# Kernel tuning notes

Hardware: AMD Instinct MI355X
Metric: run time of the kernel (lower is better)

Reference implementation:

```python
import jax, jax.numpy as jnp
import numpy as np

# LeNet C3 sparse connection table derived from the TF loop logic:
#   outputs 0-5 : 3 consecutive input channels (i, i+1, i+2 mod 6)  -> weights3[:,:,m,i]
#   outputs 6-11: 4 consecutive input channels (k..k+3 mod 6)       -> weights4[:,:,m,k]
#   outputs 12-14: channels (k, k+1, k+3, k+4 mod 6)                -> weights4_4[:,:,m,k]
#   output 15  : all 6 channels                                     -> weights6
# Missing connections contribute exactly zero, so assembling one dense
# [f,f,6,16] kernel with zeros in unconnected slots and running a single
# VALID conv computes the SAME math as the ~60 tiny conv2d calls.

BATCH, H, W, CIN, COUT, FS = 32, 512, 512, 6, 16, 5


def setup_inputs() -> dict:
    key = jax.random.key(0)
    k1, k2, k3, k4, k5, k6 = jax.random.split(key, 6)
    return {
        "inputs": jax.random.normal(k1, (BATCH, H, W, CIN), dtype=jnp.float32),
        "weights3": jax.random.normal(k2, (FS, FS, 3, 6), dtype=jnp.float32),
        "weights4": jax.random.normal(k3, (FS, FS, 4, 6), dtype=jnp.float32),
        "weights4_4": jax.random.normal(k4, (FS, FS, 4, 3), dtype=jnp.float32),
        "weights6": jax.random.normal(k5, (FS, FS, 6, 1), dtype=jnp.float32),
        "bias1": jax.random.normal(k6, (COUT,), dtype=jnp.float32),
    }


def _dense_kernel(weights3, weights4, weights4_4, weights6):
    f = weights3.shape[0]
    Wd = jnp.zeros((f, f, CIN, COUT), dtype=weights3.dtype)
    # outputs 0..5: 3 consecutive channels
    for i in range(6):
        for m in range(3):
            Wd = Wd.at[:, :, (i + m) % 6, i].set(weights3[:, :, m, i])
    # outputs 6..11: 4 consecutive channels
    for k in range(6):
        for m in range(4):
            Wd = Wd.at[:, :, (k + m) % 6, 6 + k].set(weights4[:, :, m, k])
    # outputs 12..14: offsets 0,1,3,4
    for k in range(3):
        for m, off in enumerate((0, 1, 3, 4)):
            Wd = Wd.at[:, :, (k + off) % 6, 12 + k].set(weights4_4[:, :, m, k])
    # output 15: all 6 channels
    Wd = Wd.at[:, :, :, 15].set(weights6[:, :, :, 0])
    return Wd


def reference(inputs, weights3, weights4, weights4_4, weights6, bias1):
    Wd = _dense_kernel(weights3, weights4, weights4_4, weights6)
    out = jax.lax.conv_general_dilated(
        inputs, Wd, window_strides=(1, 1), padding="VALID",
        dimension_numbers=("NHWC", "HWIO", "NHWC"))
    return out + bias1  # broadcast bias over [B, H', W', 16]
```

## Files before the change

### kernel.cpp

```cpp
#include <hip/hip_runtime.h>
#include <cstddef>

namespace {
constexpr int kBatch = 32, kH = 512, kW = 512, kCin = 6, kCout = 16, kFs = 5;
constexpr int kOH = kH - kFs + 1, kOW = kW - kFs + 1;
constexpr int kTile = 32;
constexpr int kIT = kTile + kFs - 1;
constexpr int kRowB = kIT * kCin;
constexpr int kWElems = kFs * kFs * kCin * kCout;
}

__global__ void assemble_weights(const float* __restrict__ w3,
                                 const float* __restrict__ w4,
                                 const float* __restrict__ w44,
                                 const float* __restrict__ w6,
                                 float* __restrict__ wd) {
  int i = blockIdx.x * blockDim.x + threadIdx.x;
  if (i >= kWElems) return;
  int o = i & 15;
  int c = (i >> 4) % kCin;
  int p = i / (kCout * kCin);
  float val = 0.f;
  if (o < 6) {
    int m = (c - o + 6) % 6;
    if (m < 3) val = w3[(p * 3 + m) * 6 + o];
  } else if (o < 12) {
    int k = o - 6;
    int m = (c - k + 6) % 6;
    if (m < 4) val = w4[(p * 4 + m) * 6 + k];
  } else if (o < 15) {
    int k = o - 12;
    int d = (c - k + 6) % 6;
    int m = (d == 0) ? 0 : (d == 1) ? 1 : (d == 3) ? 2 : (d == 4) ? 3 : -1;
    if (m >= 0) val = w44[(p * 4 + m) * 3 + k];
  } else {
    val = w6[p * 6 + c];
  }
  wd[i] = val;
}

#define FMA16(P)                                                                      \
  {                                                                                   \
    float v = s_in[(ty + ((P) >> 1) * 16 + ky) * kRowB + (tx + ((P)&1) * 16 + kx) * kCin + c]; \
    acc[P][0].x += v * w0.x; acc[P][0].y += v * w0.y; acc[P][0].z += v * w0.z; acc[P][0].w += v * w0.w; \
    acc[P][1].x += v * w1.x; acc[P][1].y += v * w1.y; acc[P][1].z += v * w1.z; acc[P][1].w += v * w1.w; \
    acc[P][2].x += v * w2.x; acc[P][2].y += v * w2.y; acc[P][2].z += v * w2.z; acc[P][2].w += v * w2.w; \
    acc[P][3].x += v * w3.x; acc[P][3].y += v * w3.y; acc[P][3].z += v * w3.z; acc[P][3].w += v * w3.w; \
  }

__global__ __launch_bounds__(256) void conv_sparse(
    const float* __restrict__ in, const float* __restrict__ wd,
    const float* __restrict__ bias, float* __restrict__ out) {
  __shared__ float s_in[kIT * kRowB];
  __shared__ float s_w[kWElems];

  const int t = threadIdx.x;
  const int bx0 = blockIdx.x * kTile, by0 = blockIdx.y * kTile;
  const int b = blockIdx.z;

  for (int i = t; i < kWElems; i += 256) s_w[i] = wd[i];

  const float* inb = in + (size_t)b * kH * kW * kCin;
  const bool interior = (bx0 + kIT <= kW) && (by0 + kIT <= kH);
  if (interior) {
    for (int i = t; i < kIT * kRowB; i += 256) {
      int r = i / kRowB;
      int rem = i - r * kRowB;
      s_in[i] = inb[((size_t)(by0 + r) * kW + bx0) * kCin + rem];
    }
  } else {
    for (int i = t; i < kIT * kRowB; i += 256) {
      int r = i / kRowB;
      int rem = i - r * kRowB;
      int gy = by0 + r;
      int gx = bx0 + rem / kCin;
      float v = 0.f;
      if (gy < kH && gx < kW) v = inb[((size_t)gy * kW + bx0) * kCin + rem];
      s_in[i] = v;
    }
  }
  __syncthreads();

  const int tx = t & 15, ty = t >> 4;

  const float4* bp = (const float4*)bias;
  float4 b0 = bp[0], b1 = bp[1], b2 = bp[2], b3 = bp[3];
  float4 acc[4][4];
#pragma unroll
  for (int p = 0; p < 4; ++p) {
    acc[p][0] = b0; acc[p][1] = b1; acc[p][2] = b2; acc[p][3] = b3;
  }

#pragma unroll 1
  for (int ky = 0; ky < kFs; ++ky) {
#pragma unroll
    for (int kx = 0; kx < kFs; ++kx) {
#pragma unroll
      for (int c = 0; c < kCin; ++c) {
        const float4* wp = (const float4*)&s_w[((ky * kFs + kx) * kCin + c) * kCout];
        float4 w0 = wp[0], w1 = wp[1], w2 = wp[2], w3 = wp[3];
        FMA16(0)
        FMA16(1)
        FMA16(2)
        FMA16(3)
      }
    }
  }

#pragma unroll
  for (int p = 0; p < 4; ++p) {
    int oy = by0 + ty + (p >> 1) * 16;
    int ox = bx0 + tx + (p & 1) * 16;
    if (oy < kOH && ox < kOW) {
      float4* op = (float4*)&out[(((size_t)b * kOH + oy) * kOW + ox) * kCout];
      op[0] = acc[p][0]; op[1] = acc[p][1]; op[2] = acc[p][2]; op[3] = acc[p][3];
    }
  }
}

extern "C" void kernel_launch(void* const* d_in, const int* in_sizes, int n_in,
                              void* d_out, int out_size, void* d_ws, size_t ws_size,
                              hipStream_t stream) {
  const float* in   = (const float*)d_in[0];
  const float* w3   = (const float*)d_in[1];
  const float* w4   = (const float*)d_in[2];
  const float* w44  = (const float*)d_in[3];
  const float* w6   = (const float*)d_in[4];
  const float* bias = (const float*)d_in[5];
  float* out = (float*)d_out;
  float* wd  = (float*)d_ws;

  assemble_weights<<<(kWElems + 255) / 256, 256, 0, stream>>>(w3, w4, w44, w6, wd);

  dim3 grid((kOW + kTile - 1) / kTile, (kOH + kTile - 1) / kTile, kBatch);
  conv_sparse<<<grid, 256, 0, stream>>>(in, wd, bias, out);
}
```

Measured before the change: 1.022 ms.

## Skip zero weights via static connection table and read weights from global

The inner loop now uses a compile-time per-input-channel table of the 10 connected output channels, so only the nonzero weight slots are multiplied instead of all 16. That cuts FMAs to about 60 of the original 96 per pixel and tap. Weights are now read straight from global memory (uniform scalar loads) rather than staged in shared memory. Interior input tiles are loaded as float4 and the input pairs as float2. The risks are more scalar and global weight loads inside the hot loop and possibly higher register pressure.

```diff
diff --git a/kernel.cpp b/kernel.cpp
--- a/kernel.cpp
+++ b/kernel.cpp
@@ -8,6 +8,17 @@
 constexpr int kIT = kTile + kFs - 1;
 constexpr int kRowB = kIT * kCin;
 constexpr int kWElems = kFs * kFs * kCin * kCout;
+constexpr int kRowF4 = kRowB / 4;
+constexpr int kTotF4 = kIT * kRowF4;
+
+__device__ constexpr int kSet[6][10] = {
+    {0, 4, 5, 6, 9, 10, 11, 12, 14, 15},
+    {0, 1, 5, 6, 7, 10, 11, 12, 13, 15},
+    {0, 1, 2, 6, 7, 8, 11, 13, 14, 15},
+    {1, 2, 3, 6, 7, 8, 9, 12, 14, 15},
+    {2, 3, 4, 7, 8, 9, 10, 12, 13, 15},
+    {3, 4, 5, 8, 9, 10, 11, 13, 14, 15},
+};
 }
 
 __global__ void assemble_weights(const float* __restrict__ w3,
@@ -39,34 +50,25 @@
   wd[i] = val;
 }
 
-#define FMA16(P)                                                                      \
-  {                                                                                   \
-    float v = s_in[(ty + ((P) >> 1) * 16 + ky) * kRowB + (tx + ((P)&1) * 16 + kx) * kCin + c]; \
-    acc[P][0].x += v * w0.x; acc[P][0].y += v * w0.y; acc[P][0].z += v * w0.z; acc[P][0].w += v * w0.w; \
-    acc[P][1].x += v * w1.x; acc[P][1].y += v * w1.y; acc[P][1].z += v * w1.z; acc[P][1].w += v * w1.w; \
-    acc[P][2].x += v * w2.x; acc[P][2].y += v * w2.y; acc[P][2].z += v * w2.z; acc[P][2].w += v * w2.w; \
-    acc[P][3].x += v * w3.x; acc[P][3].y += v * w3.y; acc[P][3].z += v * w3.z; acc[P][3].w += v * w3.w; \
-  }
-
 __global__ __launch_bounds__(256) void conv_sparse(
     const float* __restrict__ in, const float* __restrict__ wd,
     const float* __restrict__ bias, float* __restrict__ out) {
   __shared__ float s_in[kIT * kRowB];
-  __shared__ float s_w[kWElems];
 
   const int t = threadIdx.x;
   const int bx0 = blockIdx.x * kTile, by0 = blockIdx.y * kTile;
   const int b = blockIdx.z;
 
-  for (int i = t; i < kWElems; i += 256) s_w[i] = wd[i];
-
   const float* inb = in + (size_t)b * kH * kW * kCin;
   const bool interior = (bx0 + kIT <= kW) && (by0 + kIT <= kH);
   if (interior) {
-    for (int i = t; i < kIT * kRowB; i += 256) {
-      int r = i / kRowB;
-      int rem = i - r * kRowB;
-      s_in[i] = inb[((size_t)(by0 + r) * kW + bx0) * kCin + rem];
+    float4* s4 = (float4*)s_in;
+    for (int i = t; i < kTotF4; i += 256) {
+      int r = i / kRowF4;
+      int c4 = i - r * kRowF4;
+      const float4* g =
+          (const float4*)(inb + ((size_t)(by0 + r) * kW + bx0) * kCin);
+      s4[i] = g[c4];
     }
   } else {
     for (int i = t; i < kIT * kRowB; i += 256) {
@@ -83,26 +85,35 @@
 
   const int tx = t & 15, ty = t >> 4;
 
-  const float4* bp = (const float4*)bias;
-  float4 b0 = bp[0], b1 = bp[1], b2 = bp[2], b3 = bp[3];
-  float4 acc[4][4];
+  float acc[4][16];
 #pragma unroll
-  for (int p = 0; p < 4; ++p) {
-    acc[p][0] = b0; acc[p][1] = b1; acc[p][2] = b2; acc[p][3] = b3;
-  }
+  for (int p = 0; p < 4; ++p)
+#pragma unroll
+    for (int o = 0; o < 16; ++o) acc[p][o] = bias[o];
+
+  const int base00 = ty * kRowB + tx * kCin;
 
 #pragma unroll 1
   for (int ky = 0; ky < kFs; ++ky) {
+    const int rowb = base00 + ky * kRowB;
 #pragma unroll
     for (int kx = 0; kx < kFs; ++kx) {
 #pragma unroll
-      for (int c = 0; c < kCin; ++c) {
-        const float4* wp = (const float4*)&s_w[((ky * kFs + kx) * kCin + c) * kCout];
-        float4 w0 = wp[0], w1 = wp[1], w2 = wp[2], w3 = wp[3];
-        FMA16(0)
-        FMA16(1)
-        FMA16(2)
-        FMA16(3)
+      for (int cp = 0; cp < 3; ++cp) {
+        const int c0 = 2 * cp, c1 = 2 * cp + 1;
+        const float* w0 = &wd[((ky * kFs + kx) * kCin + c0) * kCout];
+        const float* w1 = w0 + kCout;
+#pragma unroll
+        for (int p = 0; p < 4; ++p) {
+          const float2 v = *(const float2*)&s_in[rowb + (p >> 1) * (16 * kRowB) +
+                                                 ((p & 1) * 16 + kx) * kCin + c0];
+#pragma unroll
+          for (int j = 0; j < 10; ++j)
+            acc[p][kSet[c0][j]] += v.x * w0[kSet[c0][j]];
+#pragma unroll
+          for (int j = 0; j < 10; ++j)
+            acc[p][kSet[c1][j]] += v.y * w1[kSet[c1][j]];
+        }
       }
     }
   }
@@ -113,7 +124,10 @@
     int ox = bx0 + tx + (p & 1) * 16;
     if (oy < kOH && ox < kOW) {
       float4* op = (float4*)&out[(((size_t)b * kOH + oy) * kOW + ox) * kCout];
-      op[0] = acc[p][0]; op[1] = acc[p][1]; op[2] = acc[p][2]; op[3] = acc[p][3];
+#pragma unroll
+      for (int j = 0; j < 4; ++j)
+        op[j] = make_float4(acc[p][4 * j + 0], acc[p][4 * j + 1],
+                            acc[p][4 * j + 2], acc[p][4 * j + 3]);
     }
   }
 }
```

After: 1.511 ms. 47.9% more time.
